# Kernel optimization log

Hardware: AMD Instinct MI355X
Metric: run time of the kernel (lower is better)

Reference implementation:

```python
import jax, jax.numpy as jnp
import numpy as np

N_NODES = 50000
N_EDGES = 600000
FEAT = 128
HIDDEN = 128
N_LAYERS = 3


def setup_inputs() -> dict:
    key = jax.random.key(0)
    ks = jax.random.split(key, 6)
    x = jax.random.normal(ks[0], (N_NODES, FEAT), dtype=jnp.float32)
    edge_index = jax.random.randint(ks[1], (2, N_EDGES), 0, N_NODES, dtype=jnp.int32)
    s_in = 1.0 / np.sqrt(FEAT)
    s_h = 1.0 / np.sqrt(HIDDEN)
    W_in = jax.random.uniform(ks[2], (FEAT, HIDDEN), dtype=jnp.float32, minval=-s_in, maxval=s_in)
    b_in = jax.random.uniform(ks[3], (HIDDEN,), dtype=jnp.float32, minval=-s_in, maxval=s_in)
    W_layers = jax.random.uniform(ks[4], (N_LAYERS, HIDDEN, HIDDEN), dtype=jnp.float32, minval=-s_h, maxval=s_h)
    b_layers = jax.random.uniform(ks[5], (N_LAYERS, HIDDEN), dtype=jnp.float32, minval=-s_h, maxval=s_h)
    return {"x": x, "edge_index": edge_index, "W_in": W_in, "b_in": b_in,
            "W_layers": W_layers, "b_layers": b_layers}


def reference(x, edge_index, W_in, b_in, W_layers, b_layers):
    n = x.shape[0]
    # GCNConv: add self-loops, symmetric normalization D^-1/2 (A+I) D^-1/2
    loop = jnp.arange(n, dtype=edge_index.dtype)
    src = jnp.concatenate([edge_index[0], loop])  # [E+N]
    dst = jnp.concatenate([edge_index[1], loop])  # [E+N]
    deg = jax.ops.segment_sum(jnp.ones_like(dst, dtype=x.dtype), dst, num_segments=n)
    inv_sqrt = jnp.where(deg > 0, jax.lax.rsqrt(jnp.maximum(deg, 1e-12)), 0.0)
    coeff = (inv_sqrt[src] * inv_sqrt[dst])[:, None]  # [E+N, 1]

    h = x @ W_in + b_in  # [N, H]
    for l in range(W_layers.shape[0]):
        m = h @ W_layers[l]                       # transform first (GCNConv)
        msgs = m[src] * coeff                     # gather + normalize, [E+N, H]
        agg = jax.ops.segment_sum(msgs, dst, num_segments=n) + b_layers[l]
        h = jax.nn.gelu(agg, approximate=False) + h  # exact GELU + residual
    return h
```

## Files before the change

kernel.cpp:

```cpp
#include <hip/hip_runtime.h>
#include <hip/hip_bf16.h>
#include <math.h>

#define NN 50000
#define NE 600000
#define HD 128
#define NL 3
#define TW_BLKS 64
#define GB 782
#define NRES 8
#define BPR 64
#define PBLK (NRES * BPR)
#define ECHUNK 9375
#define DRANGE 6250
#define ELLW 64
#define ZERO_OFF (NN << 8)

typedef __attribute__((ext_vector_type(8))) short short8;
typedef __attribute__((ext_vector_type(4))) float f32x4;

__device__ __forceinline__ ushort f2bf(float v) {
    union { float f; unsigned u; } c; c.f = v;
    unsigned u = c.u;
    u = (u + 0x7fffu + ((u >> 16) & 1u)) >> 16;
    return (ushort)u;
}
__device__ __forceinline__ float u2f(uint u) {
    union { uint u; float f; } c; c.u = u; return c.f;
}

__global__ __launch_bounds__(256) void init_k(const float* __restrict__ W_in,
                                              const float* __restrict__ W_layers,
                                              ushort* __restrict__ WT,
                                              ushort* __restrict__ mh) {
    int b = blockIdx.x;
    if (b == 0) {
        if (threadIdx.x < 64)
            ((uint*)(mh + (size_t)NN * HD))[threadIdx.x] = 0u;
        return;
    }
    int tloc = (b - 1) * 256 + threadIdx.x;
    #pragma unroll
    for (int q = 0; q < 4; ++q) {
        int idx = tloc + q * 16384;
        int m = idx >> 14;
        int c = (idx >> 7) & 127;
        int k = idx & 127;
        const float* W = (m == 0) ? W_in : (W_layers + (size_t)(m - 1) * HD * HD);
        WT[idx] = f2bf(W[k * HD + c]);
    }
}

template<int MODE>
__device__ __forceinline__ void gemm_body(int bid, const void* __restrict__ Av,
                                          const ushort* __restrict__ WT,
                                          const float* __restrict__ bs,
                                          ushort* __restrict__ out_b16,
                                          int nrows, ushort* swT) {
    int tid = threadIdx.x;
    #pragma unroll
    for (int i = 0; i < 8; ++i) {
        int chunk = tid + i * 256;
        int lin = chunk << 4;
        int n = lin >> 8;
        int swz = lin ^ ((n & 7) << 4);
        *(float4*)((char*)swT + swz) = *(const float4*)(WT + chunk * 8);
    }
    __syncthreads();

    int w = tid >> 6, l = tid & 63;
    int ar = l & 15, ag = l >> 4;
    int r0 = bid * 64 + w * 16;
    int arow = r0 + ar;
    bool arow_ok = arow < nrows;

    short8 afr[4];
    #pragma unroll
    for (int ks = 0; ks < 4; ++ks) {
        if (MODE == 0) {
            short8 fr = {0,0,0,0,0,0,0,0};
            if (arow_ok) {
                const float* Af = (const float*)Av;
                float4 p0 = *(const float4*)(Af + (size_t)arow * HD + ks * 32 + ag * 8);
                float4 p1 = *(const float4*)(Af + (size_t)arow * HD + ks * 32 + ag * 8 + 4);
                fr[0] = (short)f2bf(p0.x); fr[1] = (short)f2bf(p0.y);
                fr[2] = (short)f2bf(p0.z); fr[3] = (short)f2bf(p0.w);
                fr[4] = (short)f2bf(p1.x); fr[5] = (short)f2bf(p1.y);
                fr[6] = (short)f2bf(p1.z); fr[7] = (short)f2bf(p1.w);
            }
            afr[ks] = fr;
        } else {
            const ushort* Ab = (const ushort*)Av;
            afr[ks] = arow_ok ? *(const short8*)(Ab + (size_t)arow * HD + ks * 32 + ag * 8)
                              : short8{0,0,0,0,0,0,0,0};
        }
    }

    f32x4 acc[8];
    #pragma unroll
    for (int t = 0; t < 8; ++t) acc[t] = f32x4{0.f, 0.f, 0.f, 0.f};

    #pragma unroll
    for (int ks = 0; ks < 4; ++ks) {
        #pragma unroll
        for (int t = 0; t < 8; ++t) {
            int n = t * 16 + ar;
            int lin = (n << 8) + ks * 64 + ag * 16;
            int swz = lin ^ ((ar & 7) << 4);
            short8 b = *(const short8*)((const char*)swT + swz);
            acc[t] = __builtin_amdgcn_mfma_f32_16x16x32_bf16(afr[ks], b, acc[t], 0, 0, 0);
        }
    }

    #pragma unroll
    for (int q = 0; q < 4; ++q) {
        int row = r0 + ag * 4 + q;
        if (row >= nrows) continue;
        if (MODE == 0) {
            #pragma unroll
            for (int t = 0; t < 8; ++t) {
                int col = t * 16 + ar;
                out_b16[(size_t)row * HD + col] = f2bf(acc[t][q] + bs[col]);
            }
        } else {
            float s = bs[row];
            #pragma unroll
            for (int t = 0; t < 8; ++t) {
                int col = t * 16 + ar;
                out_b16[(size_t)row * HD + col] = f2bf(acc[t][q] * s);
            }
        }
    }
}

__global__ __launch_bounds__(256) void gemm0_hist_k(const float* __restrict__ x,
                                                    const ushort* __restrict__ WT,
                                                    const float* __restrict__ b_in,
                                                    ushort* __restrict__ hb,
                                                    const int* __restrict__ dst,
                                                    ushort* __restrict__ hist,
                                                    unsigned char* __restrict__ localpos) {
    __shared__ ushort swT[HD * HD];
    int blk = blockIdx.x;
    if (blk < GB) {
        gemm_body<0>(blk, x, WT, b_in, hb, NN, swT);
        return;
    }
    int p = blk - GB;
    int r = p & 7, b = p >> 3;
    int dlo = r * DRANGE;
    int* lh = (int*)swT;
    for (int i = threadIdx.x; i < DRANGE; i += 256) lh[i] = 0;
    __syncthreads();
    int base = b * ECHUNK, end = min(base + ECHUNK, NE);
    for (int eb = base + (int)threadIdx.x; eb < end; eb += 2048) {
        int dv[8];
        #pragma unroll
        for (int u = 0; u < 8; ++u) {
            int e = eb + u * 256;
            dv[u] = (e < end) ? dst[e] : -1;
        }
        #pragma unroll
        for (int u = 0; u < 8; ++u) {
            int e = eb + u * 256;
            int d = dv[u] - dlo;
            if ((unsigned)d < DRANGE) {
                int pos = atomicAdd(&lh[d], 1);
                localpos[e] = (unsigned char)min(pos, 255);
            }
        }
    }
    __syncthreads();
    ushort* hp = hist + (size_t)p * DRANGE;
    for (int i = threadIdx.x; i < DRANGE; i += 256) hp[i] = (ushort)lh[i];
}

__global__ __launch_bounds__(256) void scan_isq_k(ushort* __restrict__ hist,
                                                  int* __restrict__ cnt,
                                                  float* __restrict__ isq) {
    int r = blockIdx.x & 7;
    int d = (blockIdx.x >> 3) * 256 + threadIdx.x;
    if (d >= DRANGE) return;
    int run = 0;
    #pragma unroll 4
    for (int b = 0; b < BPR; ++b) {
        size_t idx = (size_t)((b << 3) | r) * DRANGE + d;
        int c = hist[idx];
        hist[idx] = (ushort)run;
        run += c;
    }
    int v = r * DRANGE + d;
    cnt[v] = run;
    isq[v] = rsqrtf((float)(run + 1));
}

__global__ __launch_bounds__(256) void gemm1_fill_k(const ushort* __restrict__ hb,
                                                    const ushort* __restrict__ WT1,
                                                    const float* __restrict__ isq,
                                                    ushort* __restrict__ mh,
                                                    const int* __restrict__ src,
                                                    const int* __restrict__ dst,
                                                    const ushort* __restrict__ hist,
                                                    const unsigned char* __restrict__ localpos,
                                                    int* __restrict__ ell) {
    __shared__ ushort swT[HD * HD];
    int blk = blockIdx.x;
    if (blk < GB) {
        gemm_body<1>(blk, hb, WT1, isq, mh, NN, swT);
        return;
    }
    int p = blk - GB;
    int r = p & 7, b = p >> 3;
    int dlo = r * DRANGE;
    ushort* lc = swT;
    const ushort* hp = hist + (size_t)p * DRANGE;
    for (int i = threadIdx.x; i < DRANGE; i += 256) lc[i] = hp[i];
    __syncthreads();
    int base = b * ECHUNK, end = min(base + ECHUNK, NE);
    for (int eb = base + (int)threadIdx.x; eb < end; eb += 2048) {
        int dv[8], sv[8], lp[8];
        #pragma unroll
        for (int u = 0; u < 8; ++u) {
            int e = eb + u * 256;
            bool ok = e < end;
            dv[u] = ok ? dst[e] : -1;
            sv[u] = ok ? src[e] : 0;
            lp[u] = ok ? (int)localpos[e] : 0;
        }
        #pragma unroll
        for (int u = 0; u < 8; ++u) {
            int d = dv[u] - dlo;
            if ((unsigned)d < DRANGE) {
                int slot = (int)lc[d] + lp[u];
                if (slot < ELLW)
                    ell[((size_t)(d + dlo) << 6) + slot] = sv[u] << 8;
            }
        }
    }
}

__global__ __launch_bounds__(256) void gemm_mfma_k(const ushort* __restrict__ A,
                                                   const ushort* __restrict__ WT,
                                                   const float* __restrict__ isq,
                                                   ushort* __restrict__ mh) {
    __shared__ ushort swT[HD * HD];
    gemm_body<1>(blockIdx.x, A, WT, isq, mh, NN, swT);
}

template<int LAST>
__global__ __launch_bounds__(256) void aggregate_k(const ushort* __restrict__ mh,
                                                   const int* __restrict__ cntp,
                                                   const int* __restrict__ ell,
                                                   const float* __restrict__ isq,
                                                   const float* __restrict__ bias,
                                                   float* __restrict__ h,
                                                   ushort* __restrict__ hb) {
    int gw = (int)((blockIdx.x * blockDim.x + threadIdx.x) >> 6);
    int lane = threadIdx.x & 63;
    if (gw >= NN) return;
    int v = gw;
    int cnt = min(cntp[v], ELLW);
    const char* mh_lane = (const char*)mh + lane * 4;

    uint sp = *(const uint*)(mh_lane + ((size_t)v << 8));
    float accx = u2f(sp << 16), accy = u2f(sp & 0xffff0000u);

    int offs = (lane < cnt) ? ell[(v << 6) + lane] : ZERO_OFF;
    int nb = (cnt + 15) >> 4;
    for (int b = 0; b < nb; ++b) {
        int jb = b << 4;
        int o0  = __shfl(offs, jb);
        int o1  = __shfl(offs, jb + 1);
        int o2  = __shfl(offs, jb + 2);
        int o3  = __shfl(offs, jb + 3);
        int o4  = __shfl(offs, jb + 4);
        int o5  = __shfl(offs, jb + 5);
        int o6  = __shfl(offs, jb + 6);
        int o7  = __shfl(offs, jb + 7);
        int o8  = __shfl(offs, jb + 8);
        int o9  = __shfl(offs, jb + 9);
        int o10 = __shfl(offs, jb + 10);
        int o11 = __shfl(offs, jb + 11);
        int o12 = __shfl(offs, jb + 12);
        int o13 = __shfl(offs, jb + 13);
        int o14 = __shfl(offs, jb + 14);
        int o15 = __shfl(offs, jb + 15);
        uint p0  = *(const uint*)(mh_lane + o0);
        uint p1  = *(const uint*)(mh_lane + o1);
        uint p2  = *(const uint*)(mh_lane + o2);
        uint p3  = *(const uint*)(mh_lane + o3);
        uint p4  = *(const uint*)(mh_lane + o4);
        uint p5  = *(const uint*)(mh_lane + o5);
        uint p6  = *(const uint*)(mh_lane + o6);
        uint p7  = *(const uint*)(mh_lane + o7);
        uint p8  = *(const uint*)(mh_lane + o8);
        uint p9  = *(const uint*)(mh_lane + o9);
        uint p10 = *(const uint*)(mh_lane + o10);
        uint p11 = *(const uint*)(mh_lane + o11);
        uint p12 = *(const uint*)(mh_lane + o12);
        uint p13 = *(const uint*)(mh_lane + o13);
        uint p14 = *(const uint*)(mh_lane + o14);
        uint p15 = *(const uint*)(mh_lane + o15);
        accx += u2f(p0 << 16);  accy += u2f(p0 & 0xffff0000u);
        accx += u2f(p1 << 16);  accy += u2f(p1 & 0xffff0000u);
        accx += u2f(p2 << 16);  accy += u2f(p2 & 0xffff0000u);
        accx += u2f(p3 << 16);  accy += u2f(p3 & 0xffff0000u);
        accx += u2f(p4 << 16);  accy += u2f(p4 & 0xffff0000u);
        accx += u2f(p5 << 16);  accy += u2f(p5 & 0xffff0000u);
        accx += u2f(p6 << 16);  accy += u2f(p6 & 0xffff0000u);
        accx += u2f(p7 << 16);  accy += u2f(p7 & 0xffff0000u);
        accx += u2f(p8 << 16);  accy += u2f(p8 & 0xffff0000u);
        accx += u2f(p9 << 16);  accy += u2f(p9 & 0xffff0000u);
        accx += u2f(p10 << 16); accy += u2f(p10 & 0xffff0000u);
        accx += u2f(p11 << 16); accy += u2f(p11 & 0xffff0000u);
        accx += u2f(p12 << 16); accy += u2f(p12 & 0xffff0000u);
        accx += u2f(p13 << 16); accy += u2f(p13 & 0xffff0000u);
        accx += u2f(p14 << 16); accy += u2f(p14 & 0xffff0000u);
        accx += u2f(p15 << 16); accy += u2f(p15 & 0xffff0000u);
    }

    float is = isq[v];
    float2 b = *(const float2*)&bias[lane * 2];
    float ax = accx * is + b.x;
    float ay = accy * is + b.y;
    float gx = 0.5f * ax * (1.f + erff(ax * 0.70710678118654752f));
    float gy = 0.5f * ay * (1.f + erff(ay * 0.70710678118654752f));
    uint* hbp = (uint*)((char*)hb + ((size_t)v << 8) + lane * 4);
    uint hp0 = *hbp;
    float hx = u2f(hp0 << 16) + gx;
    float hy = u2f(hp0 & 0xffff0000u) + gy;
    if (LAST) {
        *(float2*)(h + (size_t)v * HD + lane * 2) = float2{hx, hy};
    } else {
        *hbp = ((uint)f2bf(hx)) | (((uint)f2bf(hy)) << 16);
    }
}


static inline size_t align_up(size_t x, size_t a) { return (x + a - 1) & ~(a - 1); }

extern "C" void kernel_launch(void* const* d_in, const int* in_sizes, int n_in,
                              void* d_out, int out_size, void* d_ws, size_t ws_size,
                              hipStream_t stream) {
    const float* x        = (const float*)d_in[0];
    const int*   eidx     = (const int*)d_in[1];
    const float* W_in     = (const float*)d_in[2];
    const float* b_in     = (const float*)d_in[3];
    const float* W_layers = (const float*)d_in[4];
    const float* b_layers = (const float*)d_in[5];
    float* h = (float*)d_out;

    const int* src = eidx;
    const int* dst = eidx + NE;

    char* p = (char*)d_ws;
    ushort* mh = (ushort*)p;      p += align_up(sizeof(ushort) * ((size_t)NN + 1) * HD, 256);
    ushort* hb = (ushort*)p;      p += align_up(sizeof(ushort) * (size_t)NN * HD, 256);
    ushort* WT = (ushort*)p;      p += align_up(sizeof(ushort) * 4 * HD * HD, 256);
    float* isq = (float*)p;       p += align_up(sizeof(float) * NN, 256);
    int* cnt = (int*)p;           p += align_up(sizeof(int) * NN, 256);
    int* ell = (int*)p;           p += align_up(sizeof(int) * (size_t)NN * ELLW, 256);
    ushort* hist = (ushort*)p;    p += align_up(sizeof(ushort) * (size_t)PBLK * DRANGE, 256);
    unsigned char* localpos = (unsigned char*)p; p += align_up(NE, 256);

    init_k<<<1 + TW_BLKS, 256, 0, stream>>>(W_in, W_layers, WT, mh);
    gemm0_hist_k<<<GB + PBLK, 256, 0, stream>>>(x, WT, b_in, hb, dst, hist, localpos);
    scan_isq_k<<<8 * ((DRANGE + 255) / 256), 256, 0, stream>>>(hist, cnt, isq);
    gemm1_fill_k<<<GB + PBLK, 256, 0, stream>>>(hb, WT + (size_t)HD * HD, isq, mh,
                                                src, dst, hist, localpos, ell);

    for (int l = 0; l < NL; ++l) {
        if (l > 0) {
            gemm_mfma_k<<<GB, 256, 0, stream>>>(hb, WT + (size_t)(l + 1) * HD * HD,
                                                isq, mh);
        }
        if (l < NL - 1)
            aggregate_k<0><<<(NN + 3) / 4, 256, 0, stream>>>(mh, cnt, ell, isq,
                                                             b_layers + (size_t)l * HD, h, hb);
        else
            aggregate_k<1><<<(NN + 3) / 4, 256, 0, stream>>>(mh, cnt, ell, isq,
                                                             b_layers + (size_t)l * HD, h, hb);
    }
}
```

Measured before the change: 168.4 us.

## Process two row tiles per GEMM block and store ELL indices as ushort

Each GEMM block now handles two 64-row tiles, so it loads the transposed weight into shared memory once for 128 rows and the grid shrinks by half, amortising the LDS staging cost. The ELL neighbor table changes from int (pre-shifted byte offsets) to ushort node ids, halving its write and read traffic; the shift is done at load time in aggregation. The ushort ids rely on node ids fitting in 16 bits, but NN is 50000, which is below 65536. The smaller GEMM grid may reduce parallelism on a device with many CUs.

Result: slower. 173.6 us (+3.1%).

```diff
diff --git a/kernel.cpp b/kernel.cpp
--- a/kernel.cpp
+++ b/kernel.cpp
@@ -7,7 +7,8 @@
 #define HD 128
 #define NL 3
 #define TW_BLKS 64
-#define GB 782
+#define NTILES 782
+#define GGRID 391
 #define NRES 8
 #define BPR 64
 #define PBLK (NRES * BPR)
@@ -52,11 +53,11 @@
 }
 
 template<int MODE>
-__device__ __forceinline__ void gemm_body(int bid, const void* __restrict__ Av,
-                                          const ushort* __restrict__ WT,
-                                          const float* __restrict__ bs,
-                                          ushort* __restrict__ out_b16,
-                                          int nrows, ushort* swT) {
+__device__ __forceinline__ void gemm2_body(const void* __restrict__ Av,
+                                           const ushort* __restrict__ WT,
+                                           const float* __restrict__ bs,
+                                           ushort* __restrict__ out_b16,
+                                           ushort* swT) {
     int tid = threadIdx.x;
     #pragma unroll
     for (int i = 0; i < 8; ++i) {
@@ -70,64 +71,69 @@
 
     int w = tid >> 6, l = tid & 63;
     int ar = l & 15, ag = l >> 4;
-    int r0 = bid * 64 + w * 16;
-    int arow = r0 + ar;
-    bool arow_ok = arow < nrows;
-
-    short8 afr[4];
+
+    short8 afr[2][4];
     #pragma unroll
-    for (int ks = 0; ks < 4; ++ks) {
-        if (MODE == 0) {
-            short8 fr = {0,0,0,0,0,0,0,0};
-            if (arow_ok) {
-                const float* Af = (const float*)Av;
-                float4 p0 = *(const float4*)(Af + (size_t)arow * HD + ks * 32 + ag * 8);
-                float4 p1 = *(const float4*)(Af + (size_t)arow * HD + ks * 32 + ag * 8 + 4);
-                fr[0] = (short)f2bf(p0.x); fr[1] = (short)f2bf(p0.y);
-                fr[2] = (short)f2bf(p0.z); fr[3] = (short)f2bf(p0.w);
-                fr[4] = (short)f2bf(p1.x); fr[5] = (short)f2bf(p1.y);
-                fr[6] = (short)f2bf(p1.z); fr[7] = (short)f2bf(p1.w);
-            }
-            afr[ks] = fr;
-        } else {
-            const ushort* Ab = (const ushort*)Av;
-            afr[ks] = arow_ok ? *(const short8*)(Ab + (size_t)arow * HD + ks * 32 + ag * 8)
-                              : short8{0,0,0,0,0,0,0,0};
-        }
-    }
-
-    f32x4 acc[8];
+    for (int t2 = 0; t2 < 2; ++t2) {
+        int r0 = (blockIdx.x + t2 * GGRID) * 64 + w * 16;
+        int arow = r0 + ar;
+        bool ok = arow < NN;
+        #pragma unroll
+        for (int ks = 0; ks < 4; ++ks) {
+            if (MODE == 0) {
+                short8 fr = {0,0,0,0,0,0,0,0};
+                if (ok) {
+                    const float* Af = (const float*)Av;
+                    float4 p0 = *(const float4*)(Af + (size_t)arow * HD + ks * 32 + ag * 8);
+                    float4 p1 = *(const float4*)(Af + (size_t)arow * HD + ks * 32 + ag * 8 + 4);
+                    fr[0] = (short)f2bf(p0.x); fr[1] = (short)f2bf(p0.y);
+                    fr[2] = (short)f2bf(p0.z); fr[3] = (short)f2bf(p0.w);
+                    fr[4] = (short)f2bf(p1.x); fr[5] = (short)f2bf(p1.y);
+                    fr[6] = (short)f2bf(p1.z); fr[7] = (short)f2bf(p1.w);
+                }
+                afr[t2][ks] = fr;
+            } else {
+                const ushort* Ab = (const ushort*)Av;
+                afr[t2][ks] = ok ? *(const short8*)(Ab + (size_t)arow * HD + ks * 32 + ag * 8)
+                                 : short8{0,0,0,0,0,0,0,0};
+            }
+        }
+    }
+
     #pragma unroll
-    for (int t = 0; t < 8; ++t) acc[t] = f32x4{0.f, 0.f, 0.f, 0.f};
-
-    #pragma unroll
-    for (int ks = 0; ks < 4; ++ks) {
-        #pragma unroll
-        for (int t = 0; t < 8; ++t) {
-            int n = t * 16 + ar;
-            int lin = (n << 8) + ks * 64 + ag * 16;
-            int swz = lin ^ ((ar & 7) << 4);
-            short8 b = *(const short8*)((const char*)swT + swz);
-            acc[t] = __builtin_amdgcn_mfma_f32_16x16x32_bf16(afr[ks], b, acc[t], 0, 0, 0);
-        }
-    }
-
-    #pragma unroll
-    for (int q = 0; q < 4; ++q) {
-        int row = r0 + ag * 4 + q;
-        if (row >= nrows) continue;
-        if (MODE == 0) {
+    for (int t2 = 0; t2 < 2; ++t2) {
+        int r0 = (blockIdx.x + t2 * GGRID) * 64 + w * 16;
+        f32x4 acc[8];
+        #pragma unroll
+        for (int t = 0; t < 8; ++t) acc[t] = f32x4{0.f, 0.f, 0.f, 0.f};
+        #pragma unroll
+        for (int ks = 0; ks < 4; ++ks) {
             #pragma unroll
             for (int t = 0; t < 8; ++t) {
-                int col = t * 16 + ar;
-                out_b16[(size_t)row * HD + col] = f2bf(acc[t][q] + bs[col]);
-            }
-        } else {
-            float s = bs[row];
-            #pragma unroll
-            for (int t = 0; t < 8; ++t) {
-                int col = t * 16 + ar;
-                out_b16[(size_t)row * HD + col] = f2bf(acc[t][q] * s);
+                int n = t * 16 + ar;
+                int lin = (n << 8) + ks * 64 + ag * 16;
+                int swz = lin ^ ((ar & 7) << 4);
+                short8 b = *(const short8*)((const char*)swT + swz);
+                acc[t] = __builtin_amdgcn_mfma_f32_16x16x32_bf16(afr[t2][ks], b, acc[t], 0, 0, 0);
+            }
+        }
+        #pragma unroll
+        for (int q = 0; q < 4; ++q) {
+            int row = r0 + ag * 4 + q;
+            if (row >= NN) continue;
+            if (MODE == 0) {
+                #pragma unroll
+                for (int t = 0; t < 8; ++t) {
+                    int col = t * 16 + ar;
+                    out_b16[(size_t)row * HD + col] = f2bf(acc[t][q] + bs[col]);
+                }
+            } else {
+                float s = bs[row];
+                #pragma unroll
+                for (int t = 0; t < 8; ++t) {
+                    int col = t * 16 + ar;
+                    out_b16[(size_t)row * HD + col] = f2bf(acc[t][q] * s);
+                }
             }
         }
     }
@@ -142,11 +148,11 @@
                                                     unsigned char* __restrict__ localpos) {
     __shared__ ushort swT[HD * HD];
     int blk = blockIdx.x;
-    if (blk < GB) {
-        gemm_body<0>(blk, x, WT, b_in, hb, NN, swT);
+    if (blk < GGRID) {
+        gemm2_body<0>(x, WT, b_in, hb, swT);
         return;
     }
-    int p = blk - GB;
+    int p = blk - GGRID;
     int r = p & 7, b = p >> 3;
     int dlo = r * DRANGE;
     int* lh = (int*)swT;
@@ -202,14 +208,14 @@
                                                     const int* __restrict__ dst,
                                                     const ushort* __restrict__ hist,
                                                     const unsigned char* __restrict__ localpos,
-                                                    int* __restrict__ ell) {
+                                                    ushort* __restrict__ ell) {
     __shared__ ushort swT[HD * HD];
     int blk = blockIdx.x;
-    if (blk < GB) {
-        gemm_body<1>(blk, hb, WT1, isq, mh, NN, swT);
+    if (blk < GGRID) {
+        gemm2_body<1>(hb, WT1, isq, mh, swT);
         return;
     }
-    int p = blk - GB;
+    int p = blk - GGRID;
     int r = p & 7, b = p >> 3;
     int dlo = r * DRANGE;
     ushort* lc = swT;
@@ -233,7 +239,7 @@
             if ((unsigned)d < DRANGE) {
                 int slot = (int)lc[d] + lp[u];
                 if (slot < ELLW)
-                    ell[((size_t)(d + dlo) << 6) + slot] = sv[u] << 8;
+                    ell[((size_t)(d + dlo) << 6) + slot] = (ushort)sv[u];
             }
         }
     }
@@ -244,13 +250,13 @@
                                                    const float* __restrict__ isq,
                                                    ushort* __restrict__ mh) {
     __shared__ ushort swT[HD * HD];
-    gemm_body<1>(blockIdx.x, A, WT, isq, mh, NN, swT);
+    gemm2_body<1>(A, WT, isq, mh, swT);
 }
 
 template<int LAST>
 __global__ __launch_bounds__(256) void aggregate_k(const ushort* __restrict__ mh,
                                                    const int* __restrict__ cntp,
-                                                   const int* __restrict__ ell,
+                                                   const ushort* __restrict__ ell,
                                                    const float* __restrict__ isq,
                                                    const float* __restrict__ bias,
                                                    float* __restrict__ h,
@@ -265,7 +271,7 @@
     uint sp = *(const uint*)(mh_lane + ((size_t)v << 8));
     float accx = u2f(sp << 16), accy = u2f(sp & 0xffff0000u);
 
-    int offs = (lane < cnt) ? ell[(v << 6) + lane] : ZERO_OFF;
+    int offs = (lane < cnt) ? ((int)ell[(v << 6) + lane] << 8) : ZERO_OFF;
     int nb = (cnt + 15) >> 4;
     for (int b = 0; b < nb; ++b) {
         int jb = b << 4;
@@ -359,20 +365,20 @@
     ushort* WT = (ushort*)p;      p += align_up(sizeof(ushort) * 4 * HD * HD, 256);
     float* isq = (float*)p;       p += align_up(sizeof(float) * NN, 256);
     int* cnt = (int*)p;           p += align_up(sizeof(int) * NN, 256);
-    int* ell = (int*)p;           p += align_up(sizeof(int) * (size_t)NN * ELLW, 256);
+    ushort* ell = (ushort*)p;     p += align_up(sizeof(ushort) * (size_t)NN * ELLW, 256);
     ushort* hist = (ushort*)p;    p += align_up(sizeof(ushort) * (size_t)PBLK * DRANGE, 256);
     unsigned char* localpos = (unsigned char*)p; p += align_up(NE, 256);
 
     init_k<<<1 + TW_BLKS, 256, 0, stream>>>(W_in, W_layers, WT, mh);
-    gemm0_hist_k<<<GB + PBLK, 256, 0, stream>>>(x, WT, b_in, hb, dst, hist, localpos);
+    gemm0_hist_k<<<GGRID + PBLK, 256, 0, stream>>>(x, WT, b_in, hb, dst, hist, localpos);
     scan_isq_k<<<8 * ((DRANGE + 255) / 256), 256, 0, stream>>>(hist, cnt, isq);
-    gemm1_fill_k<<<GB + PBLK, 256, 0, stream>>>(hb, WT + (size_t)HD * HD, isq, mh,
-                                                src, dst, hist, localpos, ell);
+    gemm1_fill_k<<<GGRID + PBLK, 256, 0, stream>>>(hb, WT + (size_t)HD * HD, isq, mh,
+                                                   src, dst, hist, localpos, ell);
 
     for (int l = 0; l < NL; ++l) {
         if (l > 0) {
-            gemm_mfma_k<<<GB, 256, 0, stream>>>(hb, WT + (size_t)(l + 1) * HD * HD,
-                                                isq, mh);
+            gemm_mfma_k<<<GGRID, 256, 0, stream>>>(hb, WT + (size_t)(l + 1) * HD * HD,
+                                                   isq, mh);
         }
         if (l < NL - 1)
             aggregate_k<0><<<(NN + 3) / 4, 256, 0, stream>>>(mh, cnt, ell, isq,
```
